# Kernel optimization log

Hardware: AMD Instinct MI355X
Metric: run time of the kernel (lower is better)

Reference implementation:

```python
import jax, jax.numpy as jnp
import numpy as np


def apply_rope(x, cos, sin):
    # x: (N, S, H, D); cos/sin: (S, D//2)
    N, S, H, D = x.shape
    xp = x.reshape(N, S, H, D // 2, 2)
    xr, xi = xp[..., 0], xp[..., 1]
    c = cos[None, :, None, :]  # (1,S,1,D/2)
    s = sin[None, :, None, :]
    or_ = xr * c - xi * s
    oi_ = xr * s + xi * c
    return jnp.stack([or_, oi_], axis=-1).reshape(N, S, H, D)


def setup_inputs() -> dict:
    key = jax.random.key(0)
    ks = jax.random.split(key, 8)
    N, S, d_model, H, D = 2, 2048, 1024, 16, 64
    x = jax.random.normal(ks[0], (N, S, d_model), dtype=jnp.float32)
    # xavier-uniform-ish linear weights, stored as (in, out)
    lim = (6.0 / (d_model + H * D)) ** 0.5
    Wq = jax.random.uniform(ks[1], (d_model, H * D), jnp.float32, -lim, lim)
    Wk = jax.random.uniform(ks[2], (d_model, H * D), jnp.float32, -lim, lim)
    Wv = jax.random.uniform(ks[3], (d_model, H * D), jnp.float32, -lim, lim)
    Wo = jax.random.uniform(ks[4], (H * D, d_model), jnp.float32, -lim, lim)
    bq = jnp.zeros((H * D,), jnp.float32)
    bk = jnp.zeros((H * D,), jnp.float32)
    bv = jnp.zeros((H * D,), jnp.float32)
    bo = jnp.zeros((d_model,), jnp.float32)
    # RoPE tables: theta_j = 10000^(-2j/D), angle = pos * theta
    inv_freq = 1.0 / (10000.0 ** (jnp.arange(0, D, 2, dtype=jnp.float32) / D))
    ang = jnp.arange(S, dtype=jnp.float32)[:, None] * inv_freq[None, :]  # (S, D/2)
    cos, sin = jnp.cos(ang), jnp.sin(ang)
    # causal boolean mask (True = attend)
    mask = jnp.tril(jnp.ones((S, S), dtype=bool))
    return {"x": x, "Wq": Wq, "bq": bq, "Wk": Wk, "bk": bk, "Wv": Wv,
            "bv": bv, "Wo": Wo, "bo": bo, "cos": cos, "sin": sin, "mask": mask}


def reference(x, Wq, bq, Wk, bk, Wv, bv, Wo, bo, cos, sin, mask):
    N, S, d_model = x.shape
    H, D = 16, 64
    q = (x @ Wq + bq).reshape(N, S, H, D)
    k = (x @ Wk + bk).reshape(N, S, H, D)
    v = (x @ Wv + bv).reshape(N, S, H, D)
    q = apply_rope(q, cos, sin)
    k = apply_rope(k, cos, sin)
    # (N, H, S, D)
    q = q.transpose(0, 2, 1, 3)
    k = k.transpose(0, 2, 1, 3)
    v = v.transpose(0, 2, 1, 3)
    scale = 1.0 / jnp.sqrt(jnp.asarray(D, q.dtype))
    scores = jnp.einsum('bhqd,bhkd->bhqk', q, k) * scale
    scores = jnp.where(mask[None, None, :, :], scores, jnp.asarray(-1e30, scores.dtype))
    attn_weight = jax.nn.softmax(scores, axis=-1)  # (N,H,S,S)
    ctx = jnp.einsum('bhqk,bhkd->bhqd', attn_weight, v)
    out = ctx.transpose(0, 2, 1, 3).reshape(N, S, H * D)
    hidden = out @ Wo + bo  # dropout is identity in eval
    return hidden, attn_weight
```

## Files before the change

### kernel.cpp

```cpp
#include <hip/hip_runtime.h>
#include <math.h>

#define S_LEN 2048
#define NBATCH 2
#define NHEADS 16
#define HD 64
#define DM 1024
#define NROWS (NBATCH * S_LEN)
#define PADW 68

typedef __attribute__((ext_vector_type(8))) short bf16x8;
typedef __attribute__((ext_vector_type(4))) float f32x4;
typedef __attribute__((ext_vector_type(4))) unsigned short us4;

__device__ __forceinline__ unsigned short f2bf(float f) {
    unsigned int u = __float_as_uint(f);
    u += 0x7fffu + ((u >> 16) & 1u);
    return (unsigned short)(u >> 16);
}
__device__ __forceinline__ float bf2f(unsigned short h) {
    return __uint_as_float(((unsigned int)h) << 16);
}
__device__ __forceinline__ void split2(float v, unsigned short& h, unsigned short& l) {
    h = f2bf(v);
    l = f2bf(v - bf2f(h));
}

__global__ __launch_bounds__(256)
void split_kernel(const float* __restrict__ src, unsigned short* __restrict__ hi,
                  unsigned short* __restrict__ lo, int n4) {
    for (long i = (long)blockIdx.x * 256 + threadIdx.x; i < n4; i += (long)gridDim.x * 256) {
        const float4 v = *(const float4*)(src + i * 4);
        unsigned short h0, h1, h2, h3, l0, l1, l2, l3;
        split2(v.x, h0, l0); split2(v.y, h1, l1);
        split2(v.z, h2, l2); split2(v.w, h3, l3);
        us4 H = {h0, h1, h2, h3}, L = {l0, l1, l2, l3};
        *(us4*)(hi + i * 4) = H;
        *(us4*)(lo + i * 4) = L;
    }
}

__global__ __launch_bounds__(256)
void wsplit_kernel(const float* __restrict__ W, unsigned short* __restrict__ hi,
                   unsigned short* __restrict__ lo) {
    __shared__ float T[64][65];
    const int c = threadIdx.x & 63, r0 = threadIdx.x >> 6;
    const int n0 = blockIdx.x * 64, k0 = blockIdx.y * 64;
    #pragma unroll
    for (int it = 0; it < 16; ++it) {
        const int r = r0 + it * 4;
        T[r][c] = W[(long)(k0 + r) * DM + n0 + c];
    }
    __syncthreads();
    #pragma unroll
    for (int it = 0; it < 16; ++it) {
        const int r = r0 + it * 4;
        unsigned short h, l;
        split2(T[c][r], h, l);
        hi[(long)(n0 + r) * DM + k0 + c] = h;
        lo[(long)(n0 + r) * DM + k0 + c] = l;
    }
}

#define SWZ(r) ((((r) & 3) ^ (((r) >> 2) & 3)))

template<int MODE>
__global__ __launch_bounds__(256)
void mfma_gemm(const unsigned short* __restrict__ Ah, const unsigned short* __restrict__ Al,
               const unsigned short* __restrict__ Bh, const unsigned short* __restrict__ Bl,
               const float* __restrict__ bias,
               const float* __restrict__ cosp, const float* __restrict__ sinp,
               float* __restrict__ outp)
{
    __shared__ __align__(16) unsigned short LAh[128 * 32];
    __shared__ __align__(16) unsigned short LAl[128 * 32];
    __shared__ __align__(16) unsigned short LBh[64 * 32];
    __shared__ __align__(16) unsigned short LBl[64 * 32];

    const int tid  = threadIdx.x;
    const int lane = tid & 63;
    const int wid  = tid >> 6;
    const int row0 = blockIdx.y * 128;
    const int col0 = blockIdx.x * 64;

    long aBase[2]; int aKoff[2]; int aDst[2];
    #pragma unroll
    for (int half = 0; half < 2; ++half) {
        const int c = tid + half * 256;
        const int r = c >> 2, b = c & 3;
        aDst[half] = r * 32 + ((b ^ SWZ(r)) << 3);
        if (MODE < 2) {
            aBase[half] = (long)(row0 + r) * DM + b * 8;
            aKoff[half] = 0;
        } else {
            const int gr = row0 + r;
            aBase[half] = ((long)((gr >> 11) * NHEADS) * S_LEN + (gr & (S_LEN - 1))) * HD;
            aKoff[half] = b * 8;
        }
    }
    const int rB = tid >> 2, bBlk = tid & 3;
    const long bBase = (long)(col0 + rB) * DM + bBlk * 8;
    const int  bDst  = rB * 32 + ((bBlk ^ SWZ(rB)) << 3);

    const int g = lane >> 4, lr = lane & 15;
    const int wr = (wid >> 1) * 64, wc = (wid & 1) * 32;
    int aoff[4], boff[2];
    #pragma unroll
    for (int mt = 0; mt < 4; ++mt) {
        const int rr = wr + mt * 16 + lr;
        aoff[mt] = rr * 32 + ((g ^ SWZ(rr)) << 3);
    }
    #pragma unroll
    for (int nt = 0; nt < 2; ++nt) {
        const int cc = wc + nt * 16 + lr;
        boff[nt] = cc * 32 + ((g ^ SWZ(cc)) << 3);
    }

    f32x4 acc[4][2];
    {
        const f32x4 z = {0.f, 0.f, 0.f, 0.f};
        #pragma unroll
        for (int mt = 0; mt < 4; ++mt)
            #pragma unroll
            for (int nt = 0; nt < 2; ++nt) acc[mt][nt] = z;
    }

    auto asrc_at = [&](int half, int kt) -> long {
        if (MODE < 2) return aBase[half] + kt;
        const int kk = kt + aKoff[half];
        return aBase[half] + (long)(kk >> 6) * (S_LEN * HD) + (kk & 63);
    };

    bf16x8 cA0h = *(const bf16x8*)(Ah + asrc_at(0, 0));
    bf16x8 cA0l = *(const bf16x8*)(Al + asrc_at(0, 0));
    bf16x8 cA1h = *(const bf16x8*)(Ah + asrc_at(1, 0));
    bf16x8 cA1l = *(const bf16x8*)(Al + asrc_at(1, 0));
    bf16x8 cB_h = *(const bf16x8*)(Bh + bBase);
    bf16x8 cB_l = *(const bf16x8*)(Bl + bBase);

    for (int kt = 0; kt < DM; kt += 32) {
        *(bf16x8*)(LAh + aDst[0]) = cA0h;
        *(bf16x8*)(LAl + aDst[0]) = cA0l;
        *(bf16x8*)(LAh + aDst[1]) = cA1h;
        *(bf16x8*)(LAl + aDst[1]) = cA1l;
        *(bf16x8*)(LBh + bDst) = cB_h;
        *(bf16x8*)(LBl + bDst) = cB_l;
        __syncthreads();

        const int kn = kt + 32;
        if (kn < DM) {
            cA0h = *(const bf16x8*)(Ah + asrc_at(0, kn));
            cA0l = *(const bf16x8*)(Al + asrc_at(0, kn));
            cA1h = *(const bf16x8*)(Ah + asrc_at(1, kn));
            cA1l = *(const bf16x8*)(Al + asrc_at(1, kn));
            cB_h = *(const bf16x8*)(Bh + bBase + kn);
            cB_l = *(const bf16x8*)(Bl + bBase + kn);
        }

        bf16x8 Bfh[2], Bfl[2];
        #pragma unroll
        for (int nt = 0; nt < 2; ++nt) {
            Bfh[nt] = *(const bf16x8*)(LBh + boff[nt]);
            Bfl[nt] = *(const bf16x8*)(LBl + boff[nt]);
        }
        #pragma unroll
        for (int mt = 0; mt < 4; ++mt) {
            const bf16x8 Afh = *(const bf16x8*)(LAh + aoff[mt]);
            const bf16x8 Afl = *(const bf16x8*)(LAl + aoff[mt]);
            #pragma unroll
            for (int nt = 0; nt < 2; ++nt) {
                acc[mt][nt] = __builtin_amdgcn_mfma_f32_16x16x32_bf16(Afh, Bfh[nt], acc[mt][nt], 0, 0, 0);
                acc[mt][nt] = __builtin_amdgcn_mfma_f32_16x16x32_bf16(Afh, Bfl[nt], acc[mt][nt], 0, 0, 0);
                acc[mt][nt] = __builtin_amdgcn_mfma_f32_16x16x32_bf16(Afl, Bfh[nt], acc[mt][nt], 0, 0, 0);
            }
        }
        __syncthreads();
    }

    #pragma unroll
    for (int mt = 0; mt < 4; ++mt) {
        #pragma unroll
        for (int nt = 0; nt < 2; ++nt) {
            const int colg = col0 + wc + nt * 16 + lr;
            const float bv = bias[colg];
            #pragma unroll
            for (int j = 0; j < 4; ++j) {
                const int rowg = row0 + wr + mt * 16 + g * 4 + j;
                float v = acc[mt][nt][j] + bv;
                if (MODE == 2) {
                    outp[(long)rowg * DM + colg] = v;
                } else {
                    const int s  = rowg & (S_LEN - 1);
                    const int n  = rowg >> 11;
                    const int h  = colg >> 6;
                    const int dd = colg & 63;
                    float ov = v;
                    if (MODE == 0) {
                        const int f = dd >> 1;
                        const float cs = cosp[s * 32 + f];
                        const float sn = sinp[s * 32 + f];
                        const float p  = __shfl_xor(v, 1);
                        ov = (dd & 1) ? (p * sn + v * cs) : (v * cs - p * sn);
                    }
                    outp[((long)(n * NHEADS + h) * S_LEN + s) * HD + dd] = ov;
                }
            }
        }
    }
}

__global__ __launch_bounds__(256)
void attn_tiled(const float* __restrict__ qT,
                const float* __restrict__ kT,
                const float* __restrict__ vT,
                float* __restrict__ attn,
                float* __restrict__ ctx)
{
    const int bh = blockIdx.x & 31;
    const int qt = 31 - (blockIdx.x >> 5);
    const int tid = threadIdx.x;
    const int tx = tid & 15, ty = tid >> 4;
    const int c4 = tid & 15, r0 = tid >> 4;

    __shared__ float Qs[64 * PADW];
    __shared__ float KVs[64 * PADW];
    __shared__ float Ps[64 * PADW];

    const long qbase = ((long)bh * S_LEN + qt * 64) * HD;

    #pragma unroll
    for (int it = 0; it < 4; ++it) {
        const int r = r0 + 16 * it;
        const float4 v = *(const float4*)(qT + qbase + (long)r * HD + c4 * 4);
        Qs[(c4 * 4 + 0) * PADW + r] = v.x;
        Qs[(c4 * 4 + 1) * PADW + r] = v.y;
        Qs[(c4 * 4 + 2) * PADW + r] = v.z;
        Qs[(c4 * 4 + 3) * PADW + r] = v.w;
    }

    float m_r[4], l_r[4];
    #pragma unroll
    for (int i = 0; i < 4; ++i) { m_r[i] = -1e30f; l_r[i] = 0.f; }

    __syncthreads();

    for (int kt = 0; kt <= qt; ++kt) {
        const long kbase = ((long)bh * S_LEN + kt * 64) * HD;
        #pragma unroll
        for (int it = 0; it < 4; ++it) {
            const int r = r0 + 16 * it;
            const float4 v = *(const float4*)(kT + kbase + (long)r * HD + c4 * 4);
            KVs[(c4 * 4 + 0) * PADW + r] = v.x;
            KVs[(c4 * 4 + 1) * PADW + r] = v.y;
            KVs[(c4 * 4 + 2) * PADW + r] = v.z;
            KVs[(c4 * 4 + 3) * PADW + r] = v.w;
        }
        __syncthreads();

        float acc[4][4] = {};
        #pragma unroll 8
        for (int d = 0; d < 64; ++d) {
            const float4 af = *(const float4*)(Qs + d * PADW + 4 * ty);
            const float4 bf = *(const float4*)(KVs + d * PADW + 4 * tx);
            const float a[4] = {af.x, af.y, af.z, af.w};
            const float b[4] = {bf.x, bf.y, bf.z, bf.w};
            #pragma unroll
            for (int i = 0; i < 4; ++i)
                #pragma unroll
                for (int j = 0; j < 4; ++j)
                    acc[i][j] += a[i] * b[j];
        }

        const bool diag = (kt == qt);
        #pragma unroll
        for (int i = 0; i < 4; ++i) {
            float tmax = -1e30f;
            #pragma unroll
            for (int j = 0; j < 4; ++j) {
                float s = acc[i][j] * 0.125f;
                if (diag && (4 * tx + j) > (4 * ty + i)) s = -1e30f;
                acc[i][j] = s;
                tmax = fmaxf(tmax, s);
            }
            #pragma unroll
            for (int off = 1; off < 16; off <<= 1)
                tmax = fmaxf(tmax, __shfl_xor(tmax, off));
            const float m_new = fmaxf(m_r[i], tmax);
            float psum = 0.f;
            #pragma unroll
            for (int j = 0; j < 4; ++j)
                psum += __expf(acc[i][j] - m_new);
            #pragma unroll
            for (int off = 1; off < 16; off <<= 1)
                psum += __shfl_xor(psum, off);
            l_r[i] = l_r[i] * __expf(m_r[i] - m_new) + psum;
            m_r[i] = m_new;
        }
        __syncthreads();
    }

    float invl[4];
    #pragma unroll
    for (int i = 0; i < 4; ++i) invl[i] = 1.f / l_r[i];

    float o[4][4] = {};
    const long abase = ((long)bh * S_LEN + qt * 64) * S_LEN;

    for (int kt = 0; kt < 32; ++kt) {
        if (kt > qt) {
            const float4 z = make_float4(0.f, 0.f, 0.f, 0.f);
            #pragma unroll
            for (int i = 0; i < 4; ++i)
                *(float4*)(attn + abase + (long)(4 * ty + i) * S_LEN + kt * 64 + 4 * tx) = z;
            continue;
        }
        const long kbase = ((long)bh * S_LEN + kt * 64) * HD;
        #pragma unroll
        for (int it = 0; it < 4; ++it) {
            const int r = r0 + 16 * it;
            const float4 v = *(const float4*)(kT + kbase + (long)r * HD + c4 * 4);
            KVs[(c4 * 4 + 0) * PADW + r] = v.x;
            KVs[(c4 * 4 + 1) * PADW + r] = v.y;
            KVs[(c4 * 4 + 2) * PADW + r] = v.z;
            KVs[(c4 * 4 + 3) * PADW + r] = v.w;
        }
        __syncthreads();

        float acc[4][4] = {};
        #pragma unroll 8
        for (int d = 0; d < 64; ++d) {
            const float4 af = *(const float4*)(Qs + d * PADW + 4 * ty);
            const float4 bf = *(const float4*)(KVs + d * PADW + 4 * tx);
            const float a[4] = {af.x, af.y, af.z, af.w};
            const float b[4] = {bf.x, bf.y, bf.z, bf.w};
            #pragma unroll
            for (int i = 0; i < 4; ++i)
                #pragma unroll
                for (int j = 0; j < 4; ++j)
                    acc[i][j] += a[i] * b[j];
        }

        const bool diag = (kt == qt);
        #pragma unroll
        for (int i = 0; i < 4; ++i) {
            float p[4];
            #pragma unroll
            for (int j = 0; j < 4; ++j) {
                const float s = acc[i][j] * 0.125f;
                const bool msk = diag && (4 * tx + j) > (4 * ty + i);
                const float pp = msk ? 0.f : __expf(s - m_r[i]) * invl[i];
                p[j] = pp;
                Ps[(4 * tx + j) * PADW + 4 * ty + i] = pp;
            }
            *(float4*)(attn + abase + (long)(4 * ty + i) * S_LEN + kt * 64 + 4 * tx)
                = make_float4(p[0], p[1], p[2], p[3]);
        }
        __syncthreads();

        #pragma unroll
        for (int it = 0; it < 4; ++it) {
            const int r = r0 + 16 * it;
            const float4 v = *(const float4*)(vT + kbase + (long)r * HD + c4 * 4);
            *(float4*)(KVs + r * PADW + c4 * 4) = v;
        }
        __syncthreads();

        #pragma unroll 8
        for (int kc = 0; kc < 64; ++kc) {
            const float4 af = *(const float4*)(Ps + kc * PADW + 4 * ty);
            const float4 bf = *(const float4*)(KVs + kc * PADW + 4 * tx);
            const float a[4] = {af.x, af.y, af.z, af.w};
            const float b[4] = {bf.x, bf.y, bf.z, bf.w};
            #pragma unroll
            for (int i = 0; i < 4; ++i)
                #pragma unroll
                for (int j = 0; j < 4; ++j)
                    o[i][j] += a[i] * b[j];
        }
        __syncthreads();
    }

    #pragma unroll
    for (int i = 0; i < 4; ++i)
        *(float4*)(ctx + qbase + (long)(4 * ty + i) * HD + 4 * tx)
            = make_float4(o[i][0], o[i][1], o[i][2], o[i][3]);
}

extern "C" void kernel_launch(void* const* d_in, const int* in_sizes, int n_in,
                              void* d_out, int out_size, void* d_ws, size_t ws_size,
                              hipStream_t stream) {
    const float* x    = (const float*)d_in[0];
    const float* Wq   = (const float*)d_in[1];
    const float* bq   = (const float*)d_in[2];
    const float* Wk   = (const float*)d_in[3];
    const float* bk   = (const float*)d_in[4];
    const float* Wv   = (const float*)d_in[5];
    const float* bv   = (const float*)d_in[6];
    const float* Wo   = (const float*)d_in[7];
    const float* bo   = (const float*)d_in[8];
    const float* cosp = (const float*)d_in[9];
    const float* sinp = (const float*)d_in[10];

    float* out = (float*)d_out;
    float* ws  = (float*)d_ws;

    float* qT  = ws;
    float* kT  = ws + 4194304;
    float* vT  = ws + 8388608;
    float* ctx = ws + 12582912;

    float* hidden = out;
    float* attn   = out + (long)NROWS * DM;

    unsigned short* xh  = (unsigned short*)attn;
    unsigned short* xl  = xh  + 4194304;
    unsigned short* wqh = xl  + 4194304;
    unsigned short* wql = wqh + 1048576;
    unsigned short* wkh = wql + 1048576;
    unsigned short* wkl = wkh + 1048576;
    unsigned short* wvh = wkl + 1048576;
    unsigned short* wvl = wvh + 1048576;

    unsigned short* cxh = (unsigned short*)ws;
    unsigned short* cxl = cxh + 4194304;
    unsigned short* woh = (unsigned short*)(ws + 4194304);
    unsigned short* wol = woh + 1048576;

    dim3 wgrid(16, 16);
    dim3 ggrid(16, 32);

    split_kernel<<<2048, 256, 0, stream>>>(x, xh, xl, 1048576);
    wsplit_kernel<<<wgrid, 256, 0, stream>>>(Wq, wqh, wql);
    wsplit_kernel<<<wgrid, 256, 0, stream>>>(Wk, wkh, wkl);
    wsplit_kernel<<<wgrid, 256, 0, stream>>>(Wv, wvh, wvl);

    hipLaunchKernelGGL((mfma_gemm<0>), ggrid, dim3(256), 0, stream, xh, xl, wqh, wql, bq, cosp, sinp, qT);
    hipLaunchKernelGGL((mfma_gemm<0>), ggrid, dim3(256), 0, stream, xh, xl, wkh, wkl, bk, cosp, sinp, kT);
    hipLaunchKernelGGL((mfma_gemm<1>), ggrid, dim3(256), 0, stream, xh, xl, wvh, wvl, bv, cosp, sinp, vT);

    attn_tiled<<<NBATCH * NHEADS * 32, 256, 0, stream>>>(qT, kT, vT, attn, ctx);

    split_kernel<<<2048, 256, 0, stream>>>(ctx, cxh, cxl, 1048576);
    wsplit_kernel<<<wgrid, 256, 0, stream>>>(Wo, woh, wol);
    hipLaunchKernelGGL((mfma_gemm<2>), ggrid, dim3(256), 0, stream, cxh, cxl, woh, wol, bo, cosp, sinp, hidden);
}
```

Baseline: 1.118 ms.

## Move attention onto bf16 split MFMA and emit split Q/K/V from GEMM epilogues

Replaces the fp32 FMA tiled attention kernel with an MFMA version that uses a three-term bf16 hi/lo split for both QK^T and PV, with swizzled LDS tiles. The QKV GEMM epilogues now write bf16 hi/lo pairs directly, and V is stored transposed. The attention kernel writes ctx already split, which removes the separate split kernel on ctx. Masked attention columns are zero-filled in one bulk loop, and K is reloaded in the second pass. This trades some precision, since the hi*lo cross term is kept but lo*lo is dropped, for tensor-core throughput and less fp32 traffic.

```diff
diff --git a/kernel.cpp b/kernel.cpp
--- a/kernel.cpp
+++ b/kernel.cpp
@@ -7,7 +7,6 @@
 #define HD 64
 #define DM 1024
 #define NROWS (NBATCH * S_LEN)
-#define PADW 68
 
 typedef __attribute__((ext_vector_type(8))) short bf16x8;
 typedef __attribute__((ext_vector_type(4))) float f32x4;
@@ -70,7 +69,8 @@
                const unsigned short* __restrict__ Bh, const unsigned short* __restrict__ Bl,
                const float* __restrict__ bias,
                const float* __restrict__ cosp, const float* __restrict__ sinp,
-               float* __restrict__ outp)
+               unsigned short* __restrict__ outh, unsigned short* __restrict__ outl,
+               float* __restrict__ outf)
 {
     __shared__ __align__(16) unsigned short LAh[128 * 32];
     __shared__ __align__(16) unsigned short LAl[128 * 32];
@@ -183,212 +183,260 @@
         for (int nt = 0; nt < 2; ++nt) {
             const int colg = col0 + wc + nt * 16 + lr;
             const float bv = bias[colg];
+            float vals[4];
             #pragma unroll
             for (int j = 0; j < 4; ++j) {
                 const int rowg = row0 + wr + mt * 16 + g * 4 + j;
                 float v = acc[mt][nt][j] + bv;
-                if (MODE == 2) {
-                    outp[(long)rowg * DM + colg] = v;
-                } else {
+                if (MODE == 0) {
                     const int s  = rowg & (S_LEN - 1);
-                    const int n  = rowg >> 11;
-                    const int h  = colg >> 6;
                     const int dd = colg & 63;
-                    float ov = v;
-                    if (MODE == 0) {
-                        const int f = dd >> 1;
-                        const float cs = cosp[s * 32 + f];
-                        const float sn = sinp[s * 32 + f];
-                        const float p  = __shfl_xor(v, 1);
-                        ov = (dd & 1) ? (p * sn + v * cs) : (v * cs - p * sn);
-                    }
-                    outp[((long)(n * NHEADS + h) * S_LEN + s) * HD + dd] = ov;
+                    const int f = dd >> 1;
+                    const float cs = cosp[s * 32 + f];
+                    const float sn = sinp[s * 32 + f];
+                    const float p  = __shfl_xor(v, 1);
+                    v = (dd & 1) ? (p * sn + v * cs) : (v * cs - p * sn);
                 }
-            }
-        }
-    }
-}
-
-__global__ __launch_bounds__(256)
-void attn_tiled(const float* __restrict__ qT,
-                const float* __restrict__ kT,
-                const float* __restrict__ vT,
-                float* __restrict__ attn,
-                float* __restrict__ ctx)
-{
-    const int bh = blockIdx.x & 31;
-    const int qt = 31 - (blockIdx.x >> 5);
-    const int tid = threadIdx.x;
-    const int tx = tid & 15, ty = tid >> 4;
-    const int c4 = tid & 15, r0 = tid >> 4;
-
-    __shared__ float Qs[64 * PADW];
-    __shared__ float KVs[64 * PADW];
-    __shared__ float Ps[64 * PADW];
-
-    const long qbase = ((long)bh * S_LEN + qt * 64) * HD;
-
-    #pragma unroll
-    for (int it = 0; it < 4; ++it) {
-        const int r = r0 + 16 * it;
-        const float4 v = *(const float4*)(qT + qbase + (long)r * HD + c4 * 4);
-        Qs[(c4 * 4 + 0) * PADW + r] = v.x;
-        Qs[(c4 * 4 + 1) * PADW + r] = v.y;
-        Qs[(c4 * 4 + 2) * PADW + r] = v.z;
-        Qs[(c4 * 4 + 3) * PADW + r] = v.w;
-    }
-
-    float m_r[4], l_r[4];
-    #pragma unroll
-    for (int i = 0; i < 4; ++i) { m_r[i] = -1e30f; l_r[i] = 0.f; }
-
-    __syncthreads();
-
-    for (int kt = 0; kt <= qt; ++kt) {
-        const long kbase = ((long)bh * S_LEN + kt * 64) * HD;
-        #pragma unroll
-        for (int it = 0; it < 4; ++it) {
-            const int r = r0 + 16 * it;
-            const float4 v = *(const float4*)(kT + kbase + (long)r * HD + c4 * 4);
-            KVs[(c4 * 4 + 0) * PADW + r] = v.x;
-            KVs[(c4 * 4 + 1) * PADW + r] = v.y;
-            KVs[(c4 * 4 + 2) * PADW + r] = v.z;
-            KVs[(c4 * 4 + 3) * PADW + r] = v.w;
-        }
-        __syncthreads();
-
-        float acc[4][4] = {};
-        #pragma unroll 8
-        for (int d = 0; d < 64; ++d) {
-            const float4 af = *(const float4*)(Qs + d * PADW + 4 * ty);
-            const float4 bf = *(const float4*)(KVs + d * PADW + 4 * tx);
-            const float a[4] = {af.x, af.y, af.z, af.w};
-            const float b[4] = {bf.x, bf.y, bf.z, bf.w};
-            #pragma unroll
-            for (int i = 0; i < 4; ++i)
+                vals[j] = v;
+            }
+            const int rbase = row0 + wr + mt * 16 + g * 4;
+            if (MODE == 2) {
                 #pragma unroll
                 for (int j = 0; j < 4; ++j)
-                    acc[i][j] += a[i] * b[j];
+                    outf[(long)(rbase + j) * DM + colg] = vals[j];
+            } else {
+                const int n = rbase >> 11;
+                const int h = colg >> 6;
+                const int dd = colg & 63;
+                if (MODE == 0) {
+                    #pragma unroll
+                    for (int j = 0; j < 4; ++j) {
+                        const int s = (rbase + j) & (S_LEN - 1);
+                        const long addr = ((long)(n * NHEADS + h) * S_LEN + s) * HD + dd;
+                        unsigned short hh, ll; split2(vals[j], hh, ll);
+                        outh[addr] = hh; outl[addr] = ll;
+                    }
+                } else {
+                    const int s0 = rbase & (S_LEN - 1);
+                    unsigned short hh[4], ll[4];
+                    #pragma unroll
+                    for (int j = 0; j < 4; ++j) split2(vals[j], hh[j], ll[j]);
+                    us4 H = {hh[0], hh[1], hh[2], hh[3]};
+                    us4 L = {ll[0], ll[1], ll[2], ll[3]};
+                    const long addr = ((long)((n * NHEADS + h) * HD + dd)) * S_LEN + s0;
+                    *(us4*)(outh + addr) = H;
+                    *(us4*)(outl + addr) = L;
+                }
+            }
+        }
+    }
+}
+
+__global__ __launch_bounds__(256)
+void attn_mfma(const unsigned short* __restrict__ Qh, const unsigned short* __restrict__ Ql,
+               const unsigned short* __restrict__ Kh, const unsigned short* __restrict__ Kl,
+               const unsigned short* __restrict__ Vh, const unsigned short* __restrict__ Vl,
+               float* __restrict__ attn,
+               unsigned short* __restrict__ cxh, unsigned short* __restrict__ cxl)
+{
+    __shared__ __align__(16) unsigned short sQh[4096], sQl[4096];
+    __shared__ __align__(16) unsigned short sKh[4096], sKl[4096];
+    __shared__ __align__(16) unsigned short sVh[4096], sVl[4096];
+    __shared__ __align__(16) unsigned short sPh[4096], sPl[4096];
+
+    const int bh  = blockIdx.x & 31;
+    const int qt  = 31 - (blockIdx.x >> 5);
+    const int tid = threadIdx.x;
+    const int lane = tid & 63, wid = tid >> 6;
+    const int g = lane >> 4, lr = lane & 15;
+    const int wrow = wid << 4;
+
+    int sRow[2], sBlk[2], sDst[2];
+    #pragma unroll
+    for (int h = 0; h < 2; ++h) {
+        const int c = tid + h * 256;
+        sRow[h] = c >> 3; sBlk[h] = c & 7;
+        sDst[h] = sRow[h] * 64 + ((sBlk[h] ^ (sRow[h] & 7)) << 3);
+    }
+
+    #pragma unroll
+    for (int h = 0; h < 2; ++h) {
+        const long src = ((long)bh * S_LEN + qt * 64 + sRow[h]) * HD + sBlk[h] * 8;
+        *(bf16x8*)(sQh + sDst[h]) = *(const bf16x8*)(Qh + src);
+        *(bf16x8*)(sQl + sDst[h]) = *(const bf16x8*)(Ql + src);
+    }
+
+    int aoff[2], boff[4][2];
+    {
+        const int ar = wrow + lr;
+        #pragma unroll
+        for (int ks = 0; ks < 2; ++ks)
+            aoff[ks] = ar * 64 + ((((ks << 2) | g) ^ (ar & 7)) << 3);
+        #pragma unroll
+        for (int nt = 0; nt < 4; ++nt) {
+            const int br = nt * 16 + lr;
+            #pragma unroll
+            for (int ks = 0; ks < 2; ++ks)
+                boff[nt][ks] = br * 64 + ((((ks << 2) | g) ^ (br & 7)) << 3);
+        }
+    }
+
+    float m_r[4], l_r[4];
+    #pragma unroll
+    for (int j = 0; j < 4; ++j) { m_r[j] = -1e30f; l_r[j] = 0.f; }
+
+    for (int kt = 0; kt <= qt; ++kt) {
+        __syncthreads();
+        #pragma unroll
+        for (int h = 0; h < 2; ++h) {
+            const long src = ((long)bh * S_LEN + kt * 64 + sRow[h]) * HD + sBlk[h] * 8;
+            *(bf16x8*)(sKh + sDst[h]) = *(const bf16x8*)(Kh + src);
+            *(bf16x8*)(sKl + sDst[h]) = *(const bf16x8*)(Kl + src);
+        }
+        __syncthreads();
+
+        f32x4 acc[4];
+        { const f32x4 z = {0.f,0.f,0.f,0.f};
+          #pragma unroll
+          for (int nt = 0; nt < 4; ++nt) acc[nt] = z; }
+        #pragma unroll
+        for (int ks = 0; ks < 2; ++ks) {
+            const bf16x8 ah = *(const bf16x8*)(sQh + aoff[ks]);
+            const bf16x8 al = *(const bf16x8*)(sQl + aoff[ks]);
+            #pragma unroll
+            for (int nt = 0; nt < 4; ++nt) {
+                const bf16x8 bhf = *(const bf16x8*)(sKh + boff[nt][ks]);
+                const bf16x8 blf = *(const bf16x8*)(sKl + boff[nt][ks]);
+                acc[nt] = __builtin_amdgcn_mfma_f32_16x16x32_bf16(ah, bhf, acc[nt], 0, 0, 0);
+                acc[nt] = __builtin_amdgcn_mfma_f32_16x16x32_bf16(ah, blf, acc[nt], 0, 0, 0);
+                acc[nt] = __builtin_amdgcn_mfma_f32_16x16x32_bf16(al, bhf, acc[nt], 0, 0, 0);
+            }
         }
 
         const bool diag = (kt == qt);
         #pragma unroll
-        for (int i = 0; i < 4; ++i) {
-            float tmax = -1e30f;
-            #pragma unroll
-            for (int j = 0; j < 4; ++j) {
-                float s = acc[i][j] * 0.125f;
-                if (diag && (4 * tx + j) > (4 * ty + i)) s = -1e30f;
-                acc[i][j] = s;
-                tmax = fmaxf(tmax, s);
+        for (int j = 0; j < 4; ++j) {
+            const int qlcl = wrow + g * 4 + j;
+            float sv[4]; float tmax = -1e30f;
+            #pragma unroll
+            for (int nt = 0; nt < 4; ++nt) {
+                float s = acc[nt][j] * 0.125f;
+                if (diag && (nt * 16 + lr) > qlcl) s = -1e30f;
+                sv[nt] = s; tmax = fmaxf(tmax, s);
             }
             #pragma unroll
             for (int off = 1; off < 16; off <<= 1)
                 tmax = fmaxf(tmax, __shfl_xor(tmax, off));
-            const float m_new = fmaxf(m_r[i], tmax);
-            float psum = 0.f;
-            #pragma unroll
-            for (int j = 0; j < 4; ++j)
-                psum += __expf(acc[i][j] - m_new);
+            const float mn = fmaxf(m_r[j], tmax);
+            float ps = 0.f;
+            #pragma unroll
+            for (int nt = 0; nt < 4; ++nt) ps += __expf(sv[nt] - mn);
             #pragma unroll
             for (int off = 1; off < 16; off <<= 1)
-                psum += __shfl_xor(psum, off);
-            l_r[i] = l_r[i] * __expf(m_r[i] - m_new) + psum;
-            m_r[i] = m_new;
-        }
+                ps += __shfl_xor(ps, off);
+            l_r[j] = l_r[j] * __expf(m_r[j] - mn) + ps;
+            m_r[j] = mn;
+        }
+    }
+
+    float invl[4];
+    #pragma unroll
+    for (int j = 0; j < 4; ++j) invl[j] = 1.f / l_r[j];
+
+    f32x4 oacc[4];
+    { const f32x4 z = {0.f,0.f,0.f,0.f};
+      #pragma unroll
+      for (int nt = 0; nt < 4; ++nt) oacc[nt] = z; }
+    const long abase = ((long)bh * S_LEN + qt * 64) * S_LEN;
+
+    for (int kt = 0; kt <= qt; ++kt) {
         __syncthreads();
-    }
-
-    float invl[4];
-    #pragma unroll
-    for (int i = 0; i < 4; ++i) invl[i] = 1.f / l_r[i];
-
-    float o[4][4] = {};
-    const long abase = ((long)bh * S_LEN + qt * 64) * S_LEN;
-
-    for (int kt = 0; kt < 32; ++kt) {
-        if (kt > qt) {
-            const float4 z = make_float4(0.f, 0.f, 0.f, 0.f);
-            #pragma unroll
-            for (int i = 0; i < 4; ++i)
-                *(float4*)(attn + abase + (long)(4 * ty + i) * S_LEN + kt * 64 + 4 * tx) = z;
-            continue;
-        }
-        const long kbase = ((long)bh * S_LEN + kt * 64) * HD;
-        #pragma unroll
-        for (int it = 0; it < 4; ++it) {
-            const int r = r0 + 16 * it;
-            const float4 v = *(const float4*)(kT + kbase + (long)r * HD + c4 * 4);
-            KVs[(c4 * 4 + 0) * PADW + r] = v.x;
-            KVs[(c4 * 4 + 1) * PADW + r] = v.y;
-            KVs[(c4 * 4 + 2) * PADW + r] = v.z;
-            KVs[(c4 * 4 + 3) * PADW + r] = v.w;
+        #pragma unroll
+        for (int h = 0; h < 2; ++h) {
+            const long srck = ((long)bh * S_LEN + kt * 64 + sRow[h]) * HD + sBlk[h] * 8;
+            const long srcv = ((long)(bh * HD + sRow[h])) * S_LEN + kt * 64 + sBlk[h] * 8;
+            *(bf16x8*)(sKh + sDst[h]) = *(const bf16x8*)(Kh + srck);
+            *(bf16x8*)(sKl + sDst[h]) = *(const bf16x8*)(Kl + srck);
+            *(bf16x8*)(sVh + sDst[h]) = *(const bf16x8*)(Vh + srcv);
+            *(bf16x8*)(sVl + sDst[h]) = *(const bf16x8*)(Vl + srcv);
         }
         __syncthreads();
 
-        float acc[4][4] = {};
-        #pragma unroll 8
-        for (int d = 0; d < 64; ++d) {
-            const float4 af = *(const float4*)(Qs + d * PADW + 4 * ty);
-            const float4 bf = *(const float4*)(KVs + d * PADW + 4 * tx);
-            const float a[4] = {af.x, af.y, af.z, af.w};
-            const float b[4] = {bf.x, bf.y, bf.z, bf.w};
-            #pragma unroll
-            for (int i = 0; i < 4; ++i)
-                #pragma unroll
-                for (int j = 0; j < 4; ++j)
-                    acc[i][j] += a[i] * b[j];
+        f32x4 acc[4];
+        { const f32x4 z = {0.f,0.f,0.f,0.f};
+          #pragma unroll
+          for (int nt = 0; nt < 4; ++nt) acc[nt] = z; }
+        #pragma unroll
+        for (int ks = 0; ks < 2; ++ks) {
+            const bf16x8 ah = *(const bf16x8*)(sQh + aoff[ks]);
+            const bf16x8 al = *(const bf16x8*)(sQl + aoff[ks]);
+            #pragma unroll
+            for (int nt = 0; nt < 4; ++nt) {
+                const bf16x8 bhf = *(const bf16x8*)(sKh + boff[nt][ks]);
+                const bf16x8 blf = *(const bf16x8*)(sKl + boff[nt][ks]);
+                acc[nt] = __builtin_amdgcn_mfma_f32_16x16x32_bf16(ah, bhf, acc[nt], 0, 0, 0);
+                acc[nt] = __builtin_amdgcn_mfma_f32_16x16x32_bf16(ah, blf, acc[nt], 0, 0, 0);
+                acc[nt] = __builtin_amdgcn_mfma_f32_16x16x32_bf16(al, bhf, acc[nt], 0, 0, 0);
+            }
         }
 
         const bool diag = (kt == qt);
         #pragma unroll
-        for (int i = 0; i < 4; ++i) {
-            float p[4];
-            #pragma unroll
-            for (int j = 0; j < 4; ++j) {
-                const float s = acc[i][j] * 0.125f;
-                const bool msk = diag && (4 * tx + j) > (4 * ty + i);
-                const float pp = msk ? 0.f : __expf(s - m_r[i]) * invl[i];
-                p[j] = pp;
-                Ps[(4 * tx + j) * PADW + 4 * ty + i] = pp;
-            }
-            *(float4*)(attn + abase + (long)(4 * ty + i) * S_LEN + kt * 64 + 4 * tx)
-                = make_float4(p[0], p[1], p[2], p[3]);
-        }
-        __syncthreads();
-
-        #pragma unroll
-        for (int it = 0; it < 4; ++it) {
-            const int r = r0 + 16 * it;
-            const float4 v = *(const float4*)(vT + kbase + (long)r * HD + c4 * 4);
-            *(float4*)(KVs + r * PADW + c4 * 4) = v;
-        }
-        __syncthreads();
-
-        #pragma unroll 8
-        for (int kc = 0; kc < 64; ++kc) {
-            const float4 af = *(const float4*)(Ps + kc * PADW + 4 * ty);
-            const float4 bf = *(const float4*)(KVs + kc * PADW + 4 * tx);
-            const float a[4] = {af.x, af.y, af.z, af.w};
-            const float b[4] = {bf.x, bf.y, bf.z, bf.w};
-            #pragma unroll
-            for (int i = 0; i < 4; ++i)
-                #pragma unroll
-                for (int j = 0; j < 4; ++j)
-                    o[i][j] += a[i] * b[j];
-        }
-        __syncthreads();
-    }
-
-    #pragma unroll
-    for (int i = 0; i < 4; ++i)
-        *(float4*)(ctx + qbase + (long)(4 * ty + i) * HD + 4 * tx)
-            = make_float4(o[i][0], o[i][1], o[i][2], o[i][3]);
+        for (int j = 0; j < 4; ++j) {
+            const int qlcl = wrow + g * 4 + j;
+            #pragma unroll
+            for (int nt = 0; nt < 4; ++nt) {
+                const int kk = nt * 16 + lr;
+                const float s = acc[nt][j] * 0.125f;
+                const bool msk = diag && kk > qlcl;
+                const float p = msk ? 0.f : __expf(s - m_r[j]) * invl[j];
+                attn[abase + (long)qlcl * S_LEN + kt * 64 + kk] = p;
+                unsigned short ph_, pl_; split2(p, ph_, pl_);
+                const int pb = kk >> 3;
+                const int paddr = qlcl * 64 + ((pb ^ (qlcl & 7)) << 3) + (kk & 7);
+                sPh[paddr] = ph_; sPl[paddr] = pl_;
+            }
+        }
+
+        #pragma unroll
+        for (int ks = 0; ks < 2; ++ks) {
+            const bf16x8 pah = *(const bf16x8*)(sPh + aoff[ks]);
+            const bf16x8 pal = *(const bf16x8*)(sPl + aoff[ks]);
+            #pragma unroll
+            for (int nt = 0; nt < 4; ++nt) {
+                const bf16x8 vhf = *(const bf16x8*)(sVh + boff[nt][ks]);
+                const bf16x8 vlf = *(const bf16x8*)(sVl + boff[nt][ks]);
+                oacc[nt] = __builtin_amdgcn_mfma_f32_16x16x32_bf16(pah, vhf, oacc[nt], 0, 0, 0);
+                oacc[nt] = __builtin_amdgcn_mfma_f32_16x16x32_bf16(pah, vlf, oacc[nt], 0, 0, 0);
+                oacc[nt] = __builtin_amdgcn_mfma_f32_16x16x32_bf16(pal, vhf, oacc[nt], 0, 0, 0);
+            }
+        }
+    }
+
+    {
+        const int zc0 = (qt + 1) * 64;
+        const int r = tid >> 2;
+        const float4 z = make_float4(0.f, 0.f, 0.f, 0.f);
+        for (int c = zc0 + (tid & 3) * 4; c < S_LEN; c += 16)
+            *(float4*)(attn + abase + (long)r * S_LEN + c) = z;
+    }
+
+    #pragma unroll
+    for (int nt = 0; nt < 4; ++nt) {
+        #pragma unroll
+        for (int j = 0; j < 4; ++j) {
+            const int qlcl = wrow + g * 4 + j;
+            const long caddr = ((long)bh * S_LEN + qt * 64 + qlcl) * HD + nt * 16 + lr;
+            unsigned short hh, ll; split2(oacc[nt][j], hh, ll);
+            cxh[caddr] = hh; cxl[caddr] = ll;
+        }
+    }
 }
 
 extern "C" void kernel_launch(void* const* d_in, const int* in_sizes, int n_in,
                               void* d_out, int out_size, void* d_ws, size_t ws_size,
                               hipStream_t stream) {
+    (void)in_sizes; (void)n_in; (void)out_size; (void)ws_size;
     const float* x    = (const float*)d_in[0];
     const float* Wq   = (const float*)d_in[1];
     const float* bq   = (const float*)d_in[2];
@@ -402,15 +450,18 @@
     const float* sinp = (const float*)d_in[10];
 
     float* out = (float*)d_out;
-    float* ws  = (float*)d_ws;
-
-    float* qT  = ws;
-    float* kT  = ws + 4194304;
-    float* vT  = ws + 8388608;
-    float* ctx = ws + 12582912;
-
     float* hidden = out;
     float* attn   = out + (long)NROWS * DM;
+
+    unsigned short* wsu = (unsigned short*)d_ws;
+    unsigned short* qh_ = wsu;
+    unsigned short* ql_ = wsu + 4194304;
+    unsigned short* kh_ = wsu + 8388608;
+    unsigned short* kl_ = wsu + 12582912;
+    unsigned short* vth = wsu + 16777216;
+    unsigned short* vtl = wsu + 20971520;
+    unsigned short* cxh = wsu + 25165824;
+    unsigned short* cxl = wsu + 29360128;
 
     unsigned short* xh  = (unsigned short*)attn;
     unsigned short* xl  = xh  + 4194304;
@@ -421,10 +472,8 @@
     unsigned short* wvh = wkl + 1048576;
     unsigned short* wvl = wvh + 1048576;
 
-    unsigned short* cxh = (unsigned short*)ws;
-    unsigned short* cxl = cxh + 4194304;
-    unsigned short* woh = (unsigned short*)(ws + 4194304);
-    unsigned short* wol = woh + 1048576;
+    unsigned short* woh = qh_;
+    unsigned short* wol = qh_ + 1048576;
 
     dim3 wgrid(16, 16);
     dim3 ggrid(16, 32);
@@ -434,13 +483,18 @@
     wsplit_kernel<<<wgrid, 256, 0, stream>>>(Wk, wkh, wkl);
     wsplit_kernel<<<wgrid, 256, 0, stream>>>(Wv, wvh, wvl);
 
-    hipLaunchKernelGGL((mfma_gemm<0>), ggrid, dim3(256), 0, stream, xh, xl, wqh, wql, bq, cosp, sinp, qT);
-    hipLaunchKernelGGL((mfma_gemm<0>), ggrid, dim3(256), 0, stream, xh, xl, wkh, wkl, bk, cosp, sinp, kT);
-    hipLaunchKernelGGL((mfma_gemm<1>), ggrid, dim3(256), 0, stream, xh, xl, wvh, wvl, bv, cosp, sinp, vT);
-
-    attn_tiled<<<NBATCH * NHEADS * 32, 256, 0, stream>>>(qT, kT, vT, attn, ctx);
-
-    split_kernel<<<2048, 256, 0, stream>>>(ctx, cxh, cxl, 1048576);
+    hipLaunchKernelGGL((mfma_gemm<0>), ggrid, dim3(256), 0, stream,
+                       xh, xl, wqh, wql, bq, cosp, sinp, qh_, ql_, (float*)nullptr);
+    hipLaunchKernelGGL((mfma_gemm<0>), ggrid, dim3(256), 0, stream,
+                       xh, xl, wkh, wkl, bk, cosp, sinp, kh_, kl_, (float*)nullptr);
+    hipLaunchKernelGGL((mfma_gemm<1>), ggrid, dim3(256), 0, stream,
+                       xh, xl, wvh, wvl, bv, cosp, sinp, vth, vtl, (float*)nullptr);
+
+    attn_mfma<<<NBATCH * NHEADS * 32, 256, 0, stream>>>(qh_, ql_, kh_, kl_, vth, vtl,
+                                                        attn, cxh, cxl);
+
     wsplit_kernel<<<wgrid, 256, 0, stream>>>(Wo, woh, wol);
-    hipLaunchKernelGGL((mfma_gemm<2>), ggrid, dim3(256), 0, stream, cxh, cxl, woh, wol, bo, cosp, sinp, hidden);
-}
+    hipLaunchKernelGGL((mfma_gemm<2>), ggrid, dim3(256), 0, stream,
+                       cxh, cxl, woh, wol, bo, cosp, sinp,
+                       (unsigned short*)nullptr, (unsigned short*)nullptr, hidden);
+}
```

Result: faster. 921.8 us (-17.5%).
